# Optimization experiments

Hardware: AMD Instinct MI355X
Metric: run time of the kernel (lower is better)

Reference implementation:

```python
import jax, jax.numpy as jnp
import numpy as np

N_NODES = 100000
N_EDGES = 1600000
DIM = 64


def setup_inputs() -> dict:
    key = jax.random.key(0)
    k1, k2, k3 = jax.random.split(key, 3)
    x = jax.random.normal(k1, (N_NODES, DIM), dtype=jnp.float32)
    edge_index = jax.random.randint(k2, (2, N_EDGES), 0, N_NODES, dtype=jnp.int64)
    W = jax.random.normal(k3, (DIM, DIM), dtype=jnp.float32) * (1.0 / np.sqrt(DIM))
    b = jnp.zeros((DIM,), dtype=jnp.float32)
    return {"x": x, "edge_index": edge_index, "W": W, "b": b}


def reference(x, edge_index, W, b):
    # GCNConv (PyG defaults): add self-loops, symmetric normalization,
    # linear transform, scatter-add aggregation, bias; then ReLU.
    N = x.shape[0]
    loop = jnp.arange(N, dtype=edge_index.dtype)
    row = jnp.concatenate([edge_index[0], loop])  # source nodes
    col = jnp.concatenate([edge_index[1], loop])  # target nodes
    ew = jnp.ones(row.shape[0], dtype=x.dtype)

    deg = jax.ops.segment_sum(ew, col, num_segments=N)  # [N]
    dinv = jnp.where(deg > 0, jax.lax.rsqrt(deg), 0.0)
    norm = dinv[row] * ew * dinv[col]  # [E+N]

    xw = x @ W.T  # [N, D] small GEMM
    msg = norm[:, None] * xw[row]  # gather + scale, [E+N, D]
    out = jax.ops.segment_sum(msg, col, num_segments=N) + b  # scatter-add
    return jax.nn.relu(out)
```

## Files before the change

kernel.cpp:

```cpp
#include <hip/hip_runtime.h>
#include <hip/hip_bf16.h>

#define N_NODES 100000
#define N_EDGES 1600000
#define DIM 64
#define NBUCK 782
#define BK_NODES 128
#define CAP 2560
#define HA_EPB 16384
#define HA_BLOCKS 98

typedef unsigned int uint32;
typedef unsigned short ushort16;
typedef __attribute__((ext_vector_type(8))) short bf16x8;
typedef __attribute__((ext_vector_type(4))) float f32x4;

__device__ __forceinline__ float bflo(uint32 u) { return __uint_as_float(u << 16); }
__device__ __forceinline__ float bfhi(uint32 u) { return __uint_as_float(u & 0xffff0000u); }

__device__ __forceinline__ short f2bf(float f) {
    __hip_bfloat16 h = __float2bfloat16(f);
    return (short)__builtin_bit_cast(unsigned short, h);
}
__device__ __forceinline__ uint32 pack2bf(float lo, float hi) {
    unsigned short a = __builtin_bit_cast(unsigned short, __float2bfloat16(lo));
    unsigned short b = __builtin_bit_cast(unsigned short, __float2bfloat16(hi));
    return ((uint32)b << 16) | (uint32)a;
}

__global__ __launch_bounds__(1024) void init_kernel(const float* __restrict__ W,
                                                    ushort16* __restrict__ Wbf,
                                                    int* __restrict__ bcnt) {
    int i = blockIdx.x * 1024 + threadIdx.x;
    if (i < DIM * DIM)
        Wbf[i] = __builtin_bit_cast(unsigned short, __float2bfloat16(W[i]));
    if (blockIdx.x == 0 && threadIdx.x < NBUCK) bcnt[threadIdx.x] = 0;
}

__global__ __launch_bounds__(1024) void scatter_kernel(const int* __restrict__ row,
                                                       const int* __restrict__ col,
                                                       int* __restrict__ bcnt,
                                                       int* __restrict__ pairs) {
    __shared__ int h[NBUCK];
    __shared__ int base[NBUCK];
    if (threadIdx.x < NBUCK) h[threadIdx.x] = 0;
    __syncthreads();

    const int bstart = blockIdx.x * HA_EPB;
    int r[16], c[16];
#pragma unroll 16
    for (int k = 0; k < 16; ++k) {
        int e = bstart + threadIdx.x + k * 1024;
        if (e < N_EDGES) {
            r[k] = row[e];
            c[k] = col[e];
            atomicAdd(&h[c[k] >> 7], 1);
        }
    }
    __syncthreads();
    if (threadIdx.x < NBUCK) {
        int v = h[threadIdx.x];
        base[threadIdx.x] = v ? atomicAdd(&bcnt[threadIdx.x], v) : 0;
        h[threadIdx.x] = 0;
    }
    __syncthreads();
#pragma unroll 16
    for (int k = 0; k < 16; ++k) {
        int e = bstart + threadIdx.x + k * 1024;
        if (e < N_EDGES) {
            int bk = c[k] >> 7;
            int pos = base[bk] + atomicAdd(&h[bk], 1);
            if (pos < CAP) pairs[bk * CAP + pos] = (r[k] << 7) | (c[k] & 127);
        }
    }
}

__global__ __launch_bounds__(256) void sort_kernel(const int* __restrict__ bcnt,
                                                   int* __restrict__ pairs,
                                                   int* __restrict__ info,
                                                   float* __restrict__ dinv) {
    __shared__ int cnt[BK_NODES];
    __shared__ int sc[BK_NODES];
    __shared__ int cur[BK_NODES];
    __shared__ int buf[CAP];
    const int b = blockIdx.x;
    const int tid = threadIdx.x;
    int n = bcnt[b];
    if (n > CAP) n = CAP;
    if (tid < BK_NODES) cnt[tid] = 0;
    __syncthreads();
    for (int p = tid; p < n; p += 256) {
        int pk = pairs[b * CAP + p];
        buf[p] = pk;
        atomicAdd(&cnt[pk & 127], 1);
    }
    __syncthreads();
    if (tid < BK_NODES) {
        int lane = tid & 63;
        int sum = cnt[tid];
#pragma unroll
        for (int d = 1; d < 64; d <<= 1) {
            int t = __shfl_up(sum, d);
            if (lane >= d) sum += t;
        }
        sc[tid] = sum;
    }
    __syncthreads();
    if (tid >= 64 && tid < BK_NODES) sc[tid] += sc[63];
    __syncthreads();
    if (tid < BK_NODES) {
        int ex = sc[tid] - cnt[tid];
        cur[tid] = ex;
        int node = b * BK_NODES + tid;
        if (node < N_NODES) {
            info[node] = ((b * CAP + ex) << 8) | cnt[tid];
            dinv[node] = rsqrtf((float)(cnt[tid] + 1));
        }
    }
    __syncthreads();
    for (int p = tid; p < n; p += 256) {
        int pk = buf[p];
        int pos = atomicAdd(&cur[pk & 127], 1);
        pairs[b * CAP + pos] = pk >> 7;
    }
}

__global__ __launch_bounds__(256) void gemm_kernel(const float* __restrict__ x,
                                                   const ushort16* __restrict__ Wbf,
                                                   const float* __restrict__ dinv,
                                                   uint32* __restrict__ sbw) {
    __shared__ float lds[64 * 64];
    const int wave = threadIdx.x >> 6;
    const int lane = threadIdx.x & 63;
    const int base = blockIdx.x * 64;
    const int r16 = lane & 15;
    const int kb = lane >> 4;

    bf16x8 wb[4][2];
#pragma unroll
    for (int t = 0; t < 4; ++t) {
#pragma unroll
        for (int h = 0; h < 2; ++h) {
            wb[t][h] = *(const bf16x8*)&Wbf[(r16 + 16 * t) * DIM + 32 * h + kb * 8];
        }
    }

    int arow = base + wave * 16 + r16;
    if (arow >= N_NODES) arow = N_NODES - 1;
    bf16x8 af[2];
#pragma unroll
    for (int h = 0; h < 2; ++h) {
        const float* xp = &x[(size_t)arow * DIM + 32 * h + kb * 8];
        float4 p0 = *(const float4*)xp;
        float4 p1 = *(const float4*)(xp + 4);
        bf16x8 f;
        f[0] = f2bf(p0.x); f[1] = f2bf(p0.y); f[2] = f2bf(p0.z); f[3] = f2bf(p0.w);
        f[4] = f2bf(p1.x); f[5] = f2bf(p1.y); f[6] = f2bf(p1.z); f[7] = f2bf(p1.w);
        af[h] = f;
    }

    float dv[4];
#pragma unroll
    for (int i = 0; i < 4; ++i) {
        int rr = base + wave * 16 + kb * 4 + i;
        dv[i] = dinv[rr < N_NODES ? rr : N_NODES - 1];
    }

#pragma unroll
    for (int t = 0; t < 4; ++t) {
        f32x4 c = {0.0f, 0.0f, 0.0f, 0.0f};
        c = __builtin_amdgcn_mfma_f32_16x16x32_bf16(af[0], wb[t][0], c, 0, 0, 0);
        c = __builtin_amdgcn_mfma_f32_16x16x32_bf16(af[1], wb[t][1], c, 0, 0, 0);
#pragma unroll
        for (int i = 0; i < 4; ++i)
            lds[(wave * 16 + kb * 4 + i) * 64 + r16 + 16 * t] = c[i] * dv[i];
    }
    __syncthreads();

    int r = threadIdx.x >> 2;
    int cb = threadIdx.x & 3;
    int nrow = base + r;
    if (nrow < N_NODES) {
        const float* src = &lds[r * 64 + cb * 16];
        uint32 o[8];
#pragma unroll
        for (int j = 0; j < 8; ++j) {
            float2 f = *(const float2*)&src[2 * j];
            o[j] = pack2bf(f.x, f.y);
        }
        uint32* dst = sbw + (size_t)nrow * 32 + cb * 8;
        *(uint4*)dst = make_uint4(o[0], o[1], o[2], o[3]);
        *(uint4*)(dst + 4) = make_uint4(o[4], o[5], o[6], o[7]);
    }
}

__global__ __launch_bounds__(256) void agg_kernel(const int* __restrict__ info,
                                                  const int* __restrict__ srow,
                                                  const uint2* __restrict__ s4,
                                                  const float* __restrict__ dinv,
                                                  const float* __restrict__ bias,
                                                  float* __restrict__ out) {
    int n = __builtin_amdgcn_readfirstlane(blockIdx.x * 4 + (threadIdx.x >> 6));
    if (n >= N_NODES) return;
    const int lane = threadIdx.x & 63;
    const int q = lane >> 4;
    const int l = lane & 15;

    const int iv = info[n];
    const int start = iv >> 8;
    const int end = start + (iv & 255);

    float a0 = 0.0f, a1 = 0.0f, a2 = 0.0f, a3 = 0.0f;
    int p = start + q;
    for (; p + 4 < end; p += 8) {
        int r0 = srow[p];
        int r1 = srow[p + 4];
        uint2 u0 = s4[(size_t)r0 * 16 + l];
        uint2 u1 = s4[(size_t)r1 * 16 + l];
        a0 += bflo(u0.x); a1 += bfhi(u0.x); a2 += bflo(u0.y); a3 += bfhi(u0.y);
        a0 += bflo(u1.x); a1 += bfhi(u1.x); a2 += bflo(u1.y); a3 += bfhi(u1.y);
    }
    if (p < end) {
        int r0 = srow[p];
        uint2 u0 = s4[(size_t)r0 * 16 + l];
        a0 += bflo(u0.x); a1 += bfhi(u0.x); a2 += bflo(u0.y); a3 += bfhi(u0.y);
    }

    a0 += __shfl_xor(a0, 16); a1 += __shfl_xor(a1, 16);
    a2 += __shfl_xor(a2, 16); a3 += __shfl_xor(a3, 16);
    a0 += __shfl_xor(a0, 32); a1 += __shfl_xor(a1, 32);
    a2 += __shfl_xor(a2, 32); a3 += __shfl_xor(a3, 32);

    if (lane < 16) {
        uint2 us = s4[(size_t)n * 16 + l];
        a0 += bflo(us.x); a1 += bfhi(us.x); a2 += bflo(us.y); a3 += bfhi(us.y);
        float4 bb = *(const float4*)&bias[4 * l];
        float d = dinv[n];
        f32x4 o;
        o[0] = fmaxf(fmaf(d, a0, bb.x), 0.0f);
        o[1] = fmaxf(fmaf(d, a1, bb.y), 0.0f);
        o[2] = fmaxf(fmaf(d, a2, bb.z), 0.0f);
        o[3] = fmaxf(fmaf(d, a3, bb.w), 0.0f);
        __builtin_nontemporal_store(o, (f32x4*)&out[(size_t)n * DIM + 4 * l]);
    }
}

extern "C" void kernel_launch(void* const* d_in, const int* in_sizes, int n_in,
                              void* d_out, int out_size, void* d_ws, size_t ws_size,
                              hipStream_t stream) {
    const float* x    = (const float*)d_in[0];
    const int*   ei   = (const int*)d_in[1];
    const float* W    = (const float*)d_in[2];
    const float* bias = (const float*)d_in[3];
    float*       out  = (float*)d_out;

    const int* row = ei;
    const int* col = ei + N_EDGES;

    char* ws = (char*)d_ws;
    int*      bcnt  = (int*)(ws + 0);
    ushort16* Wbf   = (ushort16*)(ws + 4096);
    int*      info  = (int*)(ws + 12288);
    float*    dinv  = (float*)(ws + 412288);
    int*      pairs = (int*)(ws + 812288);
    uint32*   sbw   = (uint32*)(ws + 8819968);

    init_kernel<<<4, 1024, 0, stream>>>(W, Wbf, bcnt);
    scatter_kernel<<<HA_BLOCKS, 1024, 0, stream>>>(row, col, bcnt, pairs);
    sort_kernel<<<NBUCK, 256, 0, stream>>>(bcnt, pairs, info, dinv);
    gemm_kernel<<<(N_NODES + 63) / 64, 256, 0, stream>>>(x, Wbf, dinv, sbw);
    agg_kernel<<<(N_NODES + 3) / 4, 256, 0, stream>>>(info, pairs, (const uint2*)sbw,
                                                      dinv, bias, out);
}
```

Before: 101.2 us.

## Fuse GEMM into scatter kernel and move source dinv scaling into aggregation

The dense x@W GEMM now runs in extra blocks of the scatter kernel, so it no longer depends on dinv from the sort kernel and overlaps with edge bucketing, removing one launch. The GEMM writes unscaled bf16 results directly from MFMA registers (operands swapped to get a row-major fragment), dropping the LDS transpose. Aggregation now gathers dinv[src] per edge and applies it with fma, which adds a scattered 4-byte load per edge in exchange.

```diff
diff --git a/kernel.cpp b/kernel.cpp
--- a/kernel.cpp
+++ b/kernel.cpp
@@ -9,9 +9,9 @@
 #define CAP 2560
 #define HA_EPB 16384
 #define HA_BLOCKS 98
+#define GEMM_BLOCKS 391
 
 typedef unsigned int uint32;
-typedef unsigned short ushort16;
 typedef __attribute__((ext_vector_type(8))) short bf16x8;
 typedef __attribute__((ext_vector_type(4))) float f32x4;
 
@@ -29,7 +29,7 @@
 }
 
 __global__ __launch_bounds__(1024) void init_kernel(const float* __restrict__ W,
-                                                    ushort16* __restrict__ Wbf,
+                                                    unsigned short* __restrict__ Wbf,
                                                     int* __restrict__ bcnt) {
     int i = blockIdx.x * 1024 + threadIdx.x;
     if (i < DIM * DIM)
@@ -37,40 +37,88 @@
     if (blockIdx.x == 0 && threadIdx.x < NBUCK) bcnt[threadIdx.x] = 0;
 }
 
-__global__ __launch_bounds__(1024) void scatter_kernel(const int* __restrict__ row,
-                                                       const int* __restrict__ col,
-                                                       int* __restrict__ bcnt,
-                                                       int* __restrict__ pairs) {
+__global__ __launch_bounds__(1024) void scattergemm_kernel(
+        const int* __restrict__ row, const int* __restrict__ col,
+        int* __restrict__ bcnt, int* __restrict__ pairs,
+        const float* __restrict__ x, const unsigned short* __restrict__ Wbf,
+        uint32* __restrict__ sbw) {
     __shared__ int h[NBUCK];
     __shared__ int base[NBUCK];
-    if (threadIdx.x < NBUCK) h[threadIdx.x] = 0;
-    __syncthreads();
-
-    const int bstart = blockIdx.x * HA_EPB;
-    int r[16], c[16];
+    const int tid = threadIdx.x;
+
+    if (blockIdx.x < HA_BLOCKS) {
+        if (tid < NBUCK) h[tid] = 0;
+        __syncthreads();
+        const int bstart = blockIdx.x * HA_EPB;
+        int r[16], c[16];
 #pragma unroll 16
-    for (int k = 0; k < 16; ++k) {
-        int e = bstart + threadIdx.x + k * 1024;
-        if (e < N_EDGES) {
-            r[k] = row[e];
-            c[k] = col[e];
-            atomicAdd(&h[c[k] >> 7], 1);
-        }
-    }
-    __syncthreads();
-    if (threadIdx.x < NBUCK) {
-        int v = h[threadIdx.x];
-        base[threadIdx.x] = v ? atomicAdd(&bcnt[threadIdx.x], v) : 0;
-        h[threadIdx.x] = 0;
-    }
-    __syncthreads();
+        for (int k = 0; k < 16; ++k) {
+            int e = bstart + tid + k * 1024;
+            if (e < N_EDGES) {
+                r[k] = row[e];
+                c[k] = col[e];
+                atomicAdd(&h[c[k] >> 7], 1);
+            }
+        }
+        __syncthreads();
+        if (tid < NBUCK) {
+            int v = h[tid];
+            base[tid] = v ? atomicAdd(&bcnt[tid], v) : 0;
+            h[tid] = 0;
+        }
+        __syncthreads();
 #pragma unroll 16
-    for (int k = 0; k < 16; ++k) {
-        int e = bstart + threadIdx.x + k * 1024;
-        if (e < N_EDGES) {
-            int bk = c[k] >> 7;
-            int pos = base[bk] + atomicAdd(&h[bk], 1);
-            if (pos < CAP) pairs[bk * CAP + pos] = (r[k] << 7) | (c[k] & 127);
+        for (int k = 0; k < 16; ++k) {
+            int e = bstart + tid + k * 1024;
+            if (e < N_EDGES) {
+                int bk = c[k] >> 7;
+                int pos = base[bk] + atomicAdd(&h[bk], 1);
+                if (pos < CAP) pairs[bk * CAP + pos] = (r[k] << 7) | (c[k] & 127);
+            }
+        }
+    } else {
+        const int w = tid >> 6;
+        const int lane = tid & 63;
+        const int r16 = lane & 15;
+        const int kb = lane >> 4;
+        const int nbase = (blockIdx.x - HA_BLOCKS) * 256 + w * 16;
+
+        bf16x8 wb[4][2];
+#pragma unroll
+        for (int t = 0; t < 4; ++t) {
+#pragma unroll
+            for (int hh = 0; hh < 2; ++hh) {
+                wb[t][hh] = *(const bf16x8*)&Wbf[(r16 + 16 * t) * DIM + 32 * hh + kb * 8];
+            }
+        }
+
+        int arow = nbase + r16;
+        if (arow >= N_NODES) arow = N_NODES - 1;
+        bf16x8 af[2];
+#pragma unroll
+        for (int hh = 0; hh < 2; ++hh) {
+            const float* xp = &x[(size_t)arow * DIM + 32 * hh + kb * 8];
+            float4 p0 = *(const float4*)xp;
+            float4 p1 = *(const float4*)(xp + 4);
+            bf16x8 f;
+            f[0] = f2bf(p0.x); f[1] = f2bf(p0.y); f[2] = f2bf(p0.z); f[3] = f2bf(p0.w);
+            f[4] = f2bf(p1.x); f[5] = f2bf(p1.y); f[6] = f2bf(p1.z); f[7] = f2bf(p1.w);
+            af[hh] = f;
+        }
+
+        const int node = nbase + r16;
+        const bool valid = node < N_NODES;
+#pragma unroll
+        for (int t = 0; t < 4; ++t) {
+            f32x4 c = {0.0f, 0.0f, 0.0f, 0.0f};
+            c = __builtin_amdgcn_mfma_f32_16x16x32_bf16(wb[t][0], af[0], c, 0, 0, 0);
+            c = __builtin_amdgcn_mfma_f32_16x16x32_bf16(wb[t][1], af[1], c, 0, 0, 0);
+            if (valid) {
+                uint2 ov;
+                ov.x = pack2bf(c[0], c[1]);
+                ov.y = pack2bf(c[2], c[3]);
+                *(uint2*)&sbw[(size_t)node * 32 + t * 8 + kb * 2] = ov;
+            }
         }
     }
 }
@@ -125,75 +173,6 @@
     }
 }
 
-__global__ __launch_bounds__(256) void gemm_kernel(const float* __restrict__ x,
-                                                   const ushort16* __restrict__ Wbf,
-                                                   const float* __restrict__ dinv,
-                                                   uint32* __restrict__ sbw) {
-    __shared__ float lds[64 * 64];
-    const int wave = threadIdx.x >> 6;
-    const int lane = threadIdx.x & 63;
-    const int base = blockIdx.x * 64;
-    const int r16 = lane & 15;
-    const int kb = lane >> 4;
-
-    bf16x8 wb[4][2];
-#pragma unroll
-    for (int t = 0; t < 4; ++t) {
-#pragma unroll
-        for (int h = 0; h < 2; ++h) {
-            wb[t][h] = *(const bf16x8*)&Wbf[(r16 + 16 * t) * DIM + 32 * h + kb * 8];
-        }
-    }
-
-    int arow = base + wave * 16 + r16;
-    if (arow >= N_NODES) arow = N_NODES - 1;
-    bf16x8 af[2];
-#pragma unroll
-    for (int h = 0; h < 2; ++h) {
-        const float* xp = &x[(size_t)arow * DIM + 32 * h + kb * 8];
-        float4 p0 = *(const float4*)xp;
-        float4 p1 = *(const float4*)(xp + 4);
-        bf16x8 f;
-        f[0] = f2bf(p0.x); f[1] = f2bf(p0.y); f[2] = f2bf(p0.z); f[3] = f2bf(p0.w);
-        f[4] = f2bf(p1.x); f[5] = f2bf(p1.y); f[6] = f2bf(p1.z); f[7] = f2bf(p1.w);
-        af[h] = f;
-    }
-
-    float dv[4];
-#pragma unroll
-    for (int i = 0; i < 4; ++i) {
-        int rr = base + wave * 16 + kb * 4 + i;
-        dv[i] = dinv[rr < N_NODES ? rr : N_NODES - 1];
-    }
-
-#pragma unroll
-    for (int t = 0; t < 4; ++t) {
-        f32x4 c = {0.0f, 0.0f, 0.0f, 0.0f};
-        c = __builtin_amdgcn_mfma_f32_16x16x32_bf16(af[0], wb[t][0], c, 0, 0, 0);
-        c = __builtin_amdgcn_mfma_f32_16x16x32_bf16(af[1], wb[t][1], c, 0, 0, 0);
-#pragma unroll
-        for (int i = 0; i < 4; ++i)
-            lds[(wave * 16 + kb * 4 + i) * 64 + r16 + 16 * t] = c[i] * dv[i];
-    }
-    __syncthreads();
-
-    int r = threadIdx.x >> 2;
-    int cb = threadIdx.x & 3;
-    int nrow = base + r;
-    if (nrow < N_NODES) {
-        const float* src = &lds[r * 64 + cb * 16];
-        uint32 o[8];
-#pragma unroll
-        for (int j = 0; j < 8; ++j) {
-            float2 f = *(const float2*)&src[2 * j];
-            o[j] = pack2bf(f.x, f.y);
-        }
-        uint32* dst = sbw + (size_t)nrow * 32 + cb * 8;
-        *(uint4*)dst = make_uint4(o[0], o[1], o[2], o[3]);
-        *(uint4*)(dst + 4) = make_uint4(o[4], o[5], o[6], o[7]);
-    }
-}
-
 __global__ __launch_bounds__(256) void agg_kernel(const int* __restrict__ info,
                                                   const int* __restrict__ srow,
                                                   const uint2* __restrict__ s4,
@@ -215,15 +194,21 @@
     for (; p + 4 < end; p += 8) {
         int r0 = srow[p];
         int r1 = srow[p + 4];
+        float d0 = dinv[r0];
+        float d1 = dinv[r1];
         uint2 u0 = s4[(size_t)r0 * 16 + l];
         uint2 u1 = s4[(size_t)r1 * 16 + l];
-        a0 += bflo(u0.x); a1 += bfhi(u0.x); a2 += bflo(u0.y); a3 += bfhi(u0.y);
-        a0 += bflo(u1.x); a1 += bfhi(u1.x); a2 += bflo(u1.y); a3 += bfhi(u1.y);
+        a0 = fmaf(d0, bflo(u0.x), a0); a1 = fmaf(d0, bfhi(u0.x), a1);
+        a2 = fmaf(d0, bflo(u0.y), a2); a3 = fmaf(d0, bfhi(u0.y), a3);
+        a0 = fmaf(d1, bflo(u1.x), a0); a1 = fmaf(d1, bfhi(u1.x), a1);
+        a2 = fmaf(d1, bflo(u1.y), a2); a3 = fmaf(d1, bfhi(u1.y), a3);
     }
     if (p < end) {
         int r0 = srow[p];
+        float d0 = dinv[r0];
         uint2 u0 = s4[(size_t)r0 * 16 + l];
-        a0 += bflo(u0.x); a1 += bfhi(u0.x); a2 += bflo(u0.y); a3 += bfhi(u0.y);
+        a0 = fmaf(d0, bflo(u0.x), a0); a1 = fmaf(d0, bfhi(u0.x), a1);
+        a2 = fmaf(d0, bflo(u0.y), a2); a3 = fmaf(d0, bfhi(u0.y), a3);
     }
 
     a0 += __shfl_xor(a0, 16); a1 += __shfl_xor(a1, 16);
@@ -232,15 +217,16 @@
     a2 += __shfl_xor(a2, 32); a3 += __shfl_xor(a3, 32);
 
     if (lane < 16) {
+        float dc = dinv[n];
         uint2 us = s4[(size_t)n * 16 + l];
-        a0 += bflo(us.x); a1 += bfhi(us.x); a2 += bflo(us.y); a3 += bfhi(us.y);
+        a0 = fmaf(dc, bflo(us.x), a0); a1 = fmaf(dc, bfhi(us.x), a1);
+        a2 = fmaf(dc, bflo(us.y), a2); a3 = fmaf(dc, bfhi(us.y), a3);
         float4 bb = *(const float4*)&bias[4 * l];
-        float d = dinv[n];
         f32x4 o;
-        o[0] = fmaxf(fmaf(d, a0, bb.x), 0.0f);
-        o[1] = fmaxf(fmaf(d, a1, bb.y), 0.0f);
-        o[2] = fmaxf(fmaf(d, a2, bb.z), 0.0f);
-        o[3] = fmaxf(fmaf(d, a3, bb.w), 0.0f);
+        o[0] = fmaxf(fmaf(dc, a0, bb.x), 0.0f);
+        o[1] = fmaxf(fmaf(dc, a1, bb.y), 0.0f);
+        o[2] = fmaxf(fmaf(dc, a2, bb.z), 0.0f);
+        o[3] = fmaxf(fmaf(dc, a3, bb.w), 0.0f);
         __builtin_nontemporal_store(o, (f32x4*)&out[(size_t)n * DIM + 4 * l]);
     }
 }
@@ -258,17 +244,17 @@
     const int* col = ei + N_EDGES;
 
     char* ws = (char*)d_ws;
-    int*      bcnt  = (int*)(ws + 0);
-    ushort16* Wbf   = (ushort16*)(ws + 4096);
-    int*      info  = (int*)(ws + 12288);
-    float*    dinv  = (float*)(ws + 412288);
-    int*      pairs = (int*)(ws + 812288);
-    uint32*   sbw   = (uint32*)(ws + 8819968);
+    int*            bcnt  = (int*)(ws + 0);
+    unsigned short* Wbf   = (unsigned short*)(ws + 4096);
+    int*            info  = (int*)(ws + 12288);
+    float*          dinv  = (float*)(ws + 412288);
+    int*            pairs = (int*)(ws + 812288);
+    uint32*         sbw   = (uint32*)(ws + 8819968);
 
     init_kernel<<<4, 1024, 0, stream>>>(W, Wbf, bcnt);
-    scatter_kernel<<<HA_BLOCKS, 1024, 0, stream>>>(row, col, bcnt, pairs);
+    scattergemm_kernel<<<HA_BLOCKS + GEMM_BLOCKS, 1024, 0, stream>>>(
+        row, col, bcnt, pairs, x, Wbf, sbw);
     sort_kernel<<<NBUCK, 256, 0, stream>>>(bcnt, pairs, info, dinv);
-    gemm_kernel<<<(N_NODES + 63) / 64, 256, 0, stream>>>(x, Wbf, dinv, sbw);
     agg_kernel<<<(N_NODES + 3) / 4, 256, 0, stream>>>(info, pairs, (const uint2*)sbw,
                                                       dinv, bias, out);
 }
```

Measured after the change: 93.33 us (median of 2 runs). 7.8% less time.
